# Performance work log

Measured on AMD Instinct MI355X. Metric: run time of the kernel, lower is better.

Reference implementation:

```python
import jax, jax.numpy as jnp
import numpy as np

NUM_HEADS = 32
NUM_KV_HEADS = 8
HEAD_DIM = 128
WINDOW = 512
NUM_META = 4


def _swa_sink_mask(S):
    # allowed = causal & (within sliding window OR sink/meta token)
    i = jnp.arange(S)[:, None]   # q_idx
    j = jnp.arange(S)[None, :]   # kv_idx
    return (i >= j) & (((i - j) <= WINDOW) | (j < NUM_META))


def setup_inputs() -> dict:
    key = jax.random.key(0)
    k1, k2, k3 = jax.random.split(key, 3)
    B, S = 1, 2048
    return {
        "query_states": jax.random.normal(k1, (B, S, NUM_HEADS * HEAD_DIM), dtype=jnp.float32),
        "key_states": jax.random.normal(k2, (B, S, NUM_KV_HEADS * HEAD_DIM), dtype=jnp.float32),
        "value_states": jax.random.normal(k3, (B, S, NUM_KV_HEADS * HEAD_DIM), dtype=jnp.float32),
    }


def reference(query_states, key_states, value_states):
    B, S, _ = query_states.shape
    n_rep = NUM_HEADS // NUM_KV_HEADS
    # [B, H, S, D]
    q = query_states.reshape(B, S, NUM_HEADS, HEAD_DIM).transpose(0, 2, 1, 3)
    k = key_states.reshape(B, S, NUM_KV_HEADS, HEAD_DIM).transpose(0, 2, 1, 3)
    v = value_states.reshape(B, S, NUM_KV_HEADS, HEAD_DIM).transpose(0, 2, 1, 3)
    # repeat_kv: interleaved repeat along head dim (GQA)
    k = jnp.repeat(k, n_rep, axis=1)
    v = jnp.repeat(v, n_rep, axis=1)

    scale = 1.0 / jnp.sqrt(jnp.float32(HEAD_DIM))  # flex_attention default scale
    scores = jnp.einsum("bhqd,bhkd->bhqk", q, k) * scale
    mask = _swa_sink_mask(S)  # [S, S], every row has q_idx==kv_idx allowed
    scores = jnp.where(mask[None, None], scores, -jnp.inf)
    attn = jax.nn.softmax(scores, axis=-1)
    out = jnp.einsum("bhqk,bhkd->bhqd", attn, v)
    return out.transpose(0, 2, 1, 3).reshape(B, S, NUM_HEADS * HEAD_DIM)
```

## Files before the change

### kernel.cpp

```cpp
#include <hip/hip_runtime.h>
#include <math.h>

typedef __attribute__((ext_vector_type(8))) short bf16x8;
typedef __attribute__((ext_vector_type(16))) float f32x16;

#define WIN 512
#define META 4
#define KSTR 136
#define VSTR 72
#define QSCALE (0.08838834764831845f * 1.4426950408889634f)
#define MFIX2 20.197730572445487f

union U8 { int4 i4; bf16x8 bf; };

static __device__ __forceinline__ unsigned bf16_rne(float x) {
  unsigned u = __float_as_uint(x);
  return (u + 0x7FFFu + ((u >> 16) & 1u)) >> 16;
}
static __device__ __forceinline__ unsigned pk2_rne(float a, float b) {
  return bf16_rne(a) | (bf16_rne(b) << 16);
}
static __device__ __forceinline__ unsigned pk2_tr(float a, float b) {
  return (__float_as_uint(a) >> 16) | (__float_as_uint(b) & 0xFFFF0000u);
}

__global__ __launch_bounds__(512, 2) void swa_fused(
    const float* __restrict__ Qg, const float* __restrict__ Kg,
    const float* __restrict__ Vg, float* __restrict__ Og)
{
  __shared__ __align__(16) unsigned short Ks[2][64 * KSTR];
  __shared__ __align__(16) unsigned short Vts[2][128 * VSTR];

  const int tid = threadIdx.x;
  const int lane = tid & 63, wid = tid >> 6;
  const int cl = lane & 31, hl = lane >> 5;
  const int bid = blockIdx.x;
  const int hk = bid & 7;
  const int bq = bid >> 3;
  const int q0 = bq << 6;
  const int h = hk * 4 + (wid & 3);
  const int qw0 = q0 + ((wid >> 2) << 5);

  const int ksh = tid >> 5;
  const int ksc = (tid & 31) * 4;
  const int dgv = tid & 31;
  const int kq = tid >> 5;
  const int vchunk = 2 * (kq >> 2) + (kq & 1);
  const int vhalf  = (kq >> 1) & 1;
  const int vxor   = (dgv >> 1) & 7;

  int4 qf[8];
  {
    const float* qrow = Qg + (size_t)(qw0 + cl) * 4096 + h * 128 + hl * 8;
    #pragma unroll
    for (int kc = 0; kc < 8; ++kc) {
      float4 x = *(const float4*)(qrow + kc * 16);
      float4 y = *(const float4*)(qrow + kc * 16 + 4);
      qf[kc] = make_int4(pk2_rne(x.x*QSCALE, x.y*QSCALE), pk2_rne(x.z*QSCALE, x.w*QSCALE),
                         pk2_rne(y.x*QSCALE, y.y*QSCALE), pk2_rne(y.z*QSCALE, y.w*QSCALE));
    }
  }

  f32x16 acc[4];
  #pragma unroll
  for (int nt = 0; nt < 4; ++nt)
    #pragma unroll
    for (int i = 0; i < 16; ++i) acc[nt][i] = 0.f;
  float lpA = 0.f, lpB = 0.f;

  const int jstart = (q0 > WIN) ? ((q0 - WIN) & ~63) : 0;
  const int sink = (jstart > 0) ? 1 : 0;
  const int niter = ((q0 + 63 - jstart) >> 6) + 1 + sink;

  float4 kreg[4], vreg[4];
  {
    const int jt0 = sink ? 0 : jstart;
    const float* kb = Kg + (size_t)jt0 * 1024 + hk * 128 + ksc;
    #pragma unroll
    for (int it = 0; it < 4; ++it)
      kreg[it] = *(const float4*)(kb + (size_t)(it * 16 + ksh) * 1024);
    const float* vb = Vg + (size_t)jt0 * 1024 + hk * 128 + dgv * 4;
    #pragma unroll
    for (int i = 0; i < 4; ++i)
      vreg[i] = *(const float4*)(vb + (size_t)(4 * kq + i) * 1024);
  }

  for (int t = 0; t < niter; ++t) {
    const bool isSink = (sink != 0) && (t == 0);
    const int jt = isSink ? 0 : jstart + ((t - sink) << 6);
    const bool needMask = (jt + 63 > qw0) || (qw0 + 31 - jt > WIN);
    const int cb = t & 1;
    unsigned short* Kb = Ks[cb];
    unsigned short* Vb = Vts[cb];

    #pragma unroll
    for (int it = 0; it < 4; ++it) {
      float4 v = kreg[it];
      *(uint2*)(Kb + (it * 16 + ksh) * KSTR + ksc) =
          make_uint2(pk2_tr(v.x, v.y), pk2_tr(v.z, v.w));
    }
    #pragma unroll
    for (int e = 0; e < 4; ++e) {
      const int d = dgv * 4 + e;
      const float* f0 = (const float*)&vreg[0];
      const float* f1 = (const float*)&vreg[1];
      const float* f2 = (const float*)&vreg[2];
      const float* f3 = (const float*)&vreg[3];
      *(uint2*)(Vb + d * VSTR + ((vchunk ^ vxor) << 3) + (vhalf << 2)) =
          make_uint2(pk2_tr(f0[e], f1[e]), pk2_tr(f2[e], f3[e]));
    }
    __syncthreads();

    if (t + 1 < niter) {
      const int jn = jstart + ((t + 1 - sink) << 6);
      const float* kb = Kg + (size_t)jn * 1024 + hk * 128 + ksc;
      #pragma unroll
      for (int it = 0; it < 4; ++it)
        kreg[it] = *(const float4*)(kb + (size_t)(it * 16 + ksh) * 1024);
      const float* vb = Vg + (size_t)jn * 1024 + hk * 128 + dgv * 4;
      #pragma unroll
      for (int i = 0; i < 4; ++i)
        vreg[i] = *(const float4*)(vb + (size_t)(4 * kq + i) * 1024);
    }

    f32x16 s0v, s1v;
    #pragma unroll
    for (int i = 0; i < 16; ++i) { s0v[i] = 0.f; s1v[i] = 0.f; }
    __builtin_amdgcn_s_setprio(1);
    if (isSink) {
      #pragma unroll
      for (int kc = 0; kc < 8; ++kc) {
        U8 b; b.i4 = qf[kc];
        U8 a0; a0.i4 = *(const int4*)(Kb + cl * KSTR + kc * 16 + hl * 8);
        s0v = __builtin_amdgcn_mfma_f32_32x32x16_bf16(a0.bf, b.bf, s0v, 0, 0, 0);
      }
    } else {
      #pragma unroll
      for (int kc = 0; kc < 8; ++kc) {
        U8 b; b.i4 = qf[kc];
        U8 a0; a0.i4 = *(const int4*)(Kb + cl * KSTR + kc * 16 + hl * 8);
        s0v = __builtin_amdgcn_mfma_f32_32x32x16_bf16(a0.bf, b.bf, s0v, 0, 0, 0);
        U8 a1; a1.i4 = *(const int4*)(Kb + (32 + cl) * KSTR + kc * 16 + hl * 8);
        s1v = __builtin_amdgcn_mfma_f32_32x32x16_bf16(a1.bf, b.bf, s1v, 0, 0, 0);
      }
    }
    __builtin_amdgcn_s_setprio(0);

    unsigned pu0[16], pu1[16];
    const int q = qw0 + cl;
    #pragma unroll
    for (int ri = 0; ri < 16; ++ri) {
      const int koff = (ri & 3) + 8 * (ri >> 2) + 4 * hl;
      bool ok0 = true, ok1 = true;
      if (needMask) {
        const int k0v = jt + koff, k1v = jt + 32 + koff;
        ok0 = (q >= k0v) && (((q - k0v) <= WIN) || (k0v < META));
        ok1 = (q >= k1v) && (((q - k1v) <= WIN) || (k1v < META));
      }
      unsigned u0 = ok0 ? (__float_as_uint(__builtin_amdgcn_exp2f(s0v[ri] - MFIX2)) & 0xFFFF0000u) : 0u;
      pu0[ri] = u0;
      lpA += __uint_as_float(u0);
      if (!isSink) {
        unsigned u1 = ok1 ? (__float_as_uint(__builtin_amdgcn_exp2f(s1v[ri] - MFIX2)) & 0xFFFF0000u) : 0u;
        pu1[ri] = u1;
        lpB += __uint_as_float(u1);
      }
    }

    #define MKA(P, o) make_int4((P[(o)] >> 16) | P[(o)+1], (P[(o)+2] >> 16) | P[(o)+3], \
                                (P[(o)+4] >> 16) | P[(o)+5], (P[(o)+6] >> 16) | P[(o)+7])
    const int kcmax = isSink ? 1 : 4;
    __builtin_amdgcn_s_setprio(1);
    for (int kc = 0; kc < kcmax; ++kc) {
      U8 a;
      a.i4 = (kc == 0) ? MKA(pu0, 0) : (kc == 1) ? MKA(pu0, 8)
           : (kc == 2) ? MKA(pu1, 0) : MKA(pu1, 8);
      #pragma unroll
      for (int nt = 0; nt < 4; ++nt) {
        const int dim = nt * 32 + cl;
        U8 b; b.i4 = *(const int4*)(Vb + dim * VSTR + (((2 * kc + hl) ^ ((dim >> 3) & 7)) << 3));
        acc[nt] = __builtin_amdgcn_mfma_f32_32x32x16_bf16(a.bf, b.bf, acc[nt], 0, 0, 0);
      }
    }
    __builtin_amdgcn_s_setprio(0);
    #undef MKA
  }

  const float lp = lpA + lpB;
  const float ltot = lp + __shfl_xor(lp, 32);
  const float inv = __fdividef(1.0f, ltot);
  #pragma unroll
  for (int ri = 0; ri < 16; ++ri) {
    const int rl = (ri & 3) + 8 * (ri >> 2) + 4 * hl;
    const float invq = __shfl(inv, rl, 64);
    #pragma unroll
    for (int nt = 0; nt < 4; ++nt) {
      Og[(size_t)(qw0 + rl) * 4096 + h * 128 + nt * 32 + cl] = acc[nt][ri] * invq;
    }
  }
}

extern "C" void kernel_launch(void* const* d_in, const int* in_sizes, int n_in,
                              void* d_out, int out_size, void* d_ws, size_t ws_size,
                              hipStream_t stream) {
  const float* Q = (const float*)d_in[0];
  const float* K = (const float*)d_in[1];
  const float* V = (const float*)d_in[2];
  float* O = (float*)d_out;
  hipLaunchKernelGGL(swa_fused, dim3(256), dim3(512), 0, stream, Q, K, V, O);
}
```

Measured before the change: 122.2 us.

## Defer second half of PV MFMAs into next iteration to overlap softmax

The P·V product for the second 32-key half of each tile is moved to the start of the following iteration. It reads the previous V buffer from the double-buffered LDS, and a tail block after the loop handles the last tile. The goal is to overlap these matrix-core ops with the next tile's LDS staging and exp work, hiding latency between the QK, softmax and PV phases. P packing also switches from shift-or to a single byte-permute instruction. In exchange, the pu1 registers must stay live across iterations, which raises register pressure.

```diff
diff --git a/kernel.cpp b/kernel.cpp
--- a/kernel.cpp
+++ b/kernel.cpp
@@ -85,6 +85,16 @@
       vreg[i] = *(const float4*)(vb + (size_t)(4 * kq + i) * 1024);
   }
 
+  #define MKA(P, o) make_int4( \
+      (int)__builtin_amdgcn_perm(P[(o)+1], P[(o)+0], 0x07060302u), \
+      (int)__builtin_amdgcn_perm(P[(o)+3], P[(o)+2], 0x07060302u), \
+      (int)__builtin_amdgcn_perm(P[(o)+5], P[(o)+4], 0x07060302u), \
+      (int)__builtin_amdgcn_perm(P[(o)+7], P[(o)+6], 0x07060302u))
+
+  unsigned pu1[16];
+  #pragma unroll
+  for (int i = 0; i < 16; ++i) pu1[i] = 0u;
+
   for (int t = 0; t < niter; ++t) {
     const bool isSink = (sink != 0) && (t == 0);
     const int jt = isSink ? 0 : jstart + ((t - sink) << 6);
@@ -92,6 +102,22 @@
     const int cb = t & 1;
     unsigned short* Kb = Ks[cb];
     unsigned short* Vb = Vts[cb];
+
+    if (t > sink) {
+      const unsigned short* Vp = Vts[cb ^ 1];
+      __builtin_amdgcn_s_setprio(1);
+      #pragma unroll
+      for (int kc = 2; kc < 4; ++kc) {
+        U8 a; a.i4 = (kc == 2) ? MKA(pu1, 0) : MKA(pu1, 8);
+        #pragma unroll
+        for (int nt = 0; nt < 4; ++nt) {
+          const int dim = nt * 32 + cl;
+          U8 b; b.i4 = *(const int4*)(Vp + dim * VSTR + (((2 * kc + hl) ^ ((dim >> 3) & 7)) << 3));
+          acc[nt] = __builtin_amdgcn_mfma_f32_32x32x16_bf16(a.bf, b.bf, acc[nt], 0, 0, 0);
+        }
+      }
+      __builtin_amdgcn_s_setprio(0);
+    }
 
     #pragma unroll
     for (int it = 0; it < 4; ++it) {
@@ -146,7 +172,7 @@
     }
     __builtin_amdgcn_s_setprio(0);
 
-    unsigned pu0[16], pu1[16];
+    unsigned pu0[16];
     const int q = qw0 + cl;
     #pragma unroll
     for (int ri = 0; ri < 16; ++ri) {
@@ -167,14 +193,11 @@
       }
     }
 
-    #define MKA(P, o) make_int4((P[(o)] >> 16) | P[(o)+1], (P[(o)+2] >> 16) | P[(o)+3], \
-                                (P[(o)+4] >> 16) | P[(o)+5], (P[(o)+6] >> 16) | P[(o)+7])
-    const int kcmax = isSink ? 1 : 4;
+    const int kcmax = isSink ? 1 : 2;
     __builtin_amdgcn_s_setprio(1);
     for (int kc = 0; kc < kcmax; ++kc) {
       U8 a;
-      a.i4 = (kc == 0) ? MKA(pu0, 0) : (kc == 1) ? MKA(pu0, 8)
-           : (kc == 2) ? MKA(pu1, 0) : MKA(pu1, 8);
+      a.i4 = (kc == 0) ? MKA(pu0, 0) : MKA(pu0, 8);
       #pragma unroll
       for (int nt = 0; nt < 4; ++nt) {
         const int dim = nt * 32 + cl;
@@ -183,8 +206,22 @@
       }
     }
     __builtin_amdgcn_s_setprio(0);
-    #undef MKA
-  }
+  }
+
+  {
+    const unsigned short* Vp = Vts[(niter - 1) & 1];
+    #pragma unroll
+    for (int kc = 2; kc < 4; ++kc) {
+      U8 a; a.i4 = (kc == 2) ? MKA(pu1, 0) : MKA(pu1, 8);
+      #pragma unroll
+      for (int nt = 0; nt < 4; ++nt) {
+        const int dim = nt * 32 + cl;
+        U8 b; b.i4 = *(const int4*)(Vp + dim * VSTR + (((2 * kc + hl) ^ ((dim >> 3) & 7)) << 3));
+        acc[nt] = __builtin_amdgcn_mfma_f32_32x32x16_bf16(a.bf, b.bf, acc[nt], 0, 0, 0);
+      }
+    }
+  }
+  #undef MKA
 
   const float lp = lpA + lpB;
   const float ltot = lp + __shfl_xor(lp, 32);
```

New measurement: 122.4 us. About the same (+0.1%).

## Use 128-key tiles with two substeps and defer last PV MFMAs across barrier

Applied to the files above, without the earlier changes.

Doubles the KV tile to 128 keys per shared-memory stage, cutting the number of barriers and global-load rounds in half. Each stage is processed as two 64-key substeps, and substeps that fall entirely outside the causal or sliding-window band are skipped. The last two P·V MFMA groups of each tile are deferred into the next iteration so they overlap the next tile's shared-memory stores. P packing switches to perm instructions. The cost is double the LDS footprint and more registers for the larger K/V prefetch buffers, which could limit occupancy.

```diff
diff --git a/kernel.cpp b/kernel.cpp
--- a/kernel.cpp
+++ b/kernel.cpp
@@ -7,7 +7,7 @@
 #define WIN 512
 #define META 4
 #define KSTR 136
-#define VSTR 72
+#define VSTR 136
 #define QSCALE (0.08838834764831845f * 1.4426950408889634f)
 #define MFIX2 20.197730572445487f
 
@@ -24,11 +24,12 @@
   return (__float_as_uint(a) >> 16) | (__float_as_uint(b) & 0xFFFF0000u);
 }
 
-__global__ __launch_bounds__(512, 2) void swa_fused(
-    const float* __restrict__ Qg, const float* __restrict__ Kg,
-    const float* __restrict__ Vg, float* __restrict__ Og)
+__global__ __attribute__((amdgpu_flat_work_group_size(512, 512)))
+__attribute__((amdgpu_waves_per_eu(2, 2)))
+void swa_fused(const float* __restrict__ Qg, const float* __restrict__ Kg,
+               const float* __restrict__ Vg, float* __restrict__ Og)
 {
-  __shared__ __align__(16) unsigned short Ks[2][64 * KSTR];
+  __shared__ __align__(16) unsigned short Ks[2][128 * KSTR];
   __shared__ __align__(16) unsigned short Vts[2][128 * VSTR];
 
   const int tid = threadIdx.x;
@@ -68,122 +69,167 @@
     for (int i = 0; i < 16; ++i) acc[nt][i] = 0.f;
   float lpA = 0.f, lpB = 0.f;
 
-  const int jstart = (q0 > WIN) ? ((q0 - WIN) & ~63) : 0;
+  const int jstart = (q0 > WIN) ? ((q0 - WIN) & ~127) : 0;
   const int sink = (jstart > 0) ? 1 : 0;
-  const int niter = ((q0 + 63 - jstart) >> 6) + 1 + sink;
-
-  float4 kreg[4], vreg[4];
+  const int ntile = (q0 + 64 - jstart + 127) >> 7;
+  const int niter = ntile + sink;
+
+  auto pv4 = [&](const unsigned short* Vh, const int hb, const int kc,
+                 unsigned w0, unsigned w1, unsigned w2, unsigned w3) {
+    U8 a; a.i4 = make_int4((int)w0, (int)w1, (int)w2, (int)w3);
+    #pragma unroll
+    for (int nt = 0; nt < 4; ++nt) {
+      const int dim = nt * 32 + cl;
+      U8 b; b.i4 = *(const int4*)(Vh + dim * VSTR +
+                    ((8 * hb + ((2 * kc + hl) ^ ((dim >> 3) & 7))) << 3));
+      acc[nt] = __builtin_amdgcn_mfma_f32_32x32x16_bf16(a.bf, b.bf, acc[nt], 0, 0, 0);
+    }
+  };
+
+  unsigned pkD[8];
+  #pragma unroll
+  for (int i = 0; i < 8; ++i) pkD[i] = 0u;
+
+  auto substep = [&](const int cb, const int jts, const int hb,
+                     const bool isS, const bool defer) -> bool {
+    if (jts > qw0 + 31) return false;
+    if ((jts + 63 < qw0 - WIN) && (jts >= META)) return false;
+    const bool needMask = (jts + 63 > qw0) || (qw0 + 31 - jts > WIN);
+    const unsigned short* Kh = &Ks[cb][hb * 64 * KSTR];
+    const unsigned short* Vh = &Vts[cb][0];
+
+    f32x16 s0v, s1v;
+    #pragma unroll
+    for (int i = 0; i < 16; ++i) { s0v[i] = 0.f; s1v[i] = 0.f; }
+    __builtin_amdgcn_s_setprio(1);
+    #pragma unroll
+    for (int kc = 0; kc < 8; ++kc) {
+      U8 b; b.i4 = qf[kc];
+      U8 a0; a0.i4 = *(const int4*)(Kh + cl * KSTR + kc * 16 + hl * 8);
+      s0v = __builtin_amdgcn_mfma_f32_32x32x16_bf16(a0.bf, b.bf, s0v, 0, 0, 0);
+      if (!isS) {
+        U8 a1; a1.i4 = *(const int4*)(Kh + (32 + cl) * KSTR + kc * 16 + hl * 8);
+        s1v = __builtin_amdgcn_mfma_f32_32x32x16_bf16(a1.bf, b.bf, s1v, 0, 0, 0);
+      }
+    }
+    __builtin_amdgcn_s_setprio(0);
+
+    unsigned pk0[8], pk1[8];
+    const int q = qw0 + cl;
+    #pragma unroll
+    for (int ri = 0; ri < 16; ri += 2) {
+      const int koff = (ri & 3) + 8 * (ri >> 2) + 4 * hl;
+      bool okE = true, okO = true, okE1 = true, okO1 = true;
+      if (needMask) {
+        const int kE = jts + koff;
+        okE  = (q >= kE)     && (((q - kE)     <= WIN) || (kE     < META));
+        okO  = (q >= kE + 1) && (((q - kE - 1) <= WIN) || (kE + 1 < META));
+        const int kF = kE + 32;
+        okE1 = (q >= kF)     && (((q - kF)     <= WIN) || (kF     < META));
+        okO1 = (q >= kF + 1) && (((q - kF - 1) <= WIN) || (kF + 1 < META));
+      }
+      unsigned uE = okE ? (__float_as_uint(__builtin_amdgcn_exp2f(s0v[ri]   - MFIX2)) & 0xFFFF0000u) : 0u;
+      unsigned uO = okO ? (__float_as_uint(__builtin_amdgcn_exp2f(s0v[ri+1] - MFIX2)) & 0xFFFF0000u) : 0u;
+      lpA += __uint_as_float(uE) + __uint_as_float(uO);
+      pk0[ri >> 1] = __builtin_amdgcn_perm(uO, uE, 0x07060302u);
+      if (!isS) {
+        unsigned vE = okE1 ? (__float_as_uint(__builtin_amdgcn_exp2f(s1v[ri]   - MFIX2)) & 0xFFFF0000u) : 0u;
+        unsigned vO = okO1 ? (__float_as_uint(__builtin_amdgcn_exp2f(s1v[ri+1] - MFIX2)) & 0xFFFF0000u) : 0u;
+        lpB += __uint_as_float(vE) + __uint_as_float(vO);
+        pk1[ri >> 1] = __builtin_amdgcn_perm(vO, vE, 0x07060302u);
+      }
+    }
+
+    __builtin_amdgcn_s_setprio(1);
+    pv4(Vh, hb, 0, pk0[0], pk0[1], pk0[2], pk0[3]);
+    if (!isS) {
+      pv4(Vh, hb, 1, pk0[4], pk0[5], pk0[6], pk0[7]);
+      if (!defer) {
+        pv4(Vh, hb, 2, pk1[0], pk1[1], pk1[2], pk1[3]);
+        pv4(Vh, hb, 3, pk1[4], pk1[5], pk1[6], pk1[7]);
+      } else {
+        #pragma unroll
+        for (int j = 0; j < 8; ++j) pkD[j] = pk1[j];
+      }
+    }
+    __builtin_amdgcn_s_setprio(0);
+    return true;
+  };
+
+  float4 kreg[8], vreg[8];
   {
     const int jt0 = sink ? 0 : jstart;
     const float* kb = Kg + (size_t)jt0 * 1024 + hk * 128 + ksc;
     #pragma unroll
-    for (int it = 0; it < 4; ++it)
+    for (int it = 0; it < 8; ++it)
       kreg[it] = *(const float4*)(kb + (size_t)(it * 16 + ksh) * 1024);
     const float* vb = Vg + (size_t)jt0 * 1024 + hk * 128 + dgv * 4;
     #pragma unroll
-    for (int i = 0; i < 4; ++i)
-      vreg[i] = *(const float4*)(vb + (size_t)(4 * kq + i) * 1024);
+    for (int i = 0; i < 8; ++i)
+      vreg[i] = *(const float4*)(vb + (size_t)((i >> 2) * 64 + 4 * kq + (i & 3)) * 1024);
   }
 
   for (int t = 0; t < niter; ++t) {
-    const bool isSink = (sink != 0) && (t == 0);
-    const int jt = isSink ? 0 : jstart + ((t - sink) << 6);
-    const bool needMask = (jt + 63 > qw0) || (qw0 + 31 - jt > WIN);
+    const bool isSinkT = (sink != 0) && (t == 0);
+    const int jt = isSinkT ? 0 : jstart + ((t - sink) << 7);
     const int cb = t & 1;
-    unsigned short* Kb = Ks[cb];
-    unsigned short* Vb = Vts[cb];
-
-    #pragma unroll
-    for (int it = 0; it < 4; ++it) {
+
+    if (t > sink) {
+      const unsigned short* Vp = &Vts[cb ^ 1][0];
+      __builtin_amdgcn_s_setprio(1);
+      pv4(Vp, 1, 2, pkD[0], pkD[1], pkD[2], pkD[3]);
+      pv4(Vp, 1, 3, pkD[4], pkD[5], pkD[6], pkD[7]);
+      __builtin_amdgcn_s_setprio(0);
+    }
+
+    #pragma unroll
+    for (int it = 0; it < 8; ++it) {
       float4 v = kreg[it];
-      *(uint2*)(Kb + (it * 16 + ksh) * KSTR + ksc) =
+      *(uint2*)(&Ks[cb][(it * 16 + ksh) * KSTR + ksc]) =
           make_uint2(pk2_tr(v.x, v.y), pk2_tr(v.z, v.w));
     }
     #pragma unroll
-    for (int e = 0; e < 4; ++e) {
-      const int d = dgv * 4 + e;
-      const float* f0 = (const float*)&vreg[0];
-      const float* f1 = (const float*)&vreg[1];
-      const float* f2 = (const float*)&vreg[2];
-      const float* f3 = (const float*)&vreg[3];
-      *(uint2*)(Vb + d * VSTR + ((vchunk ^ vxor) << 3) + (vhalf << 2)) =
-          make_uint2(pk2_tr(f0[e], f1[e]), pk2_tr(f2[e], f3[e]));
+    for (int hf = 0; hf < 2; ++hf) {
+      const float* f0 = (const float*)&vreg[hf * 4 + 0];
+      const float* f1 = (const float*)&vreg[hf * 4 + 1];
+      const float* f2 = (const float*)&vreg[hf * 4 + 2];
+      const float* f3 = (const float*)&vreg[hf * 4 + 3];
+      #pragma unroll
+      for (int e = 0; e < 4; ++e) {
+        const int d = dgv * 4 + e;
+        *(uint2*)(&Vts[cb][d * VSTR + ((8 * hf + (vchunk ^ vxor)) << 3) + (vhalf << 2)]) =
+            make_uint2(pk2_tr(f0[e], f1[e]), pk2_tr(f2[e], f3[e]));
+      }
     }
     __syncthreads();
 
     if (t + 1 < niter) {
-      const int jn = jstart + ((t + 1 - sink) << 6);
+      const int jn = jstart + ((t + 1 - sink) << 7);
       const float* kb = Kg + (size_t)jn * 1024 + hk * 128 + ksc;
       #pragma unroll
-      for (int it = 0; it < 4; ++it)
+      for (int it = 0; it < 8; ++it)
         kreg[it] = *(const float4*)(kb + (size_t)(it * 16 + ksh) * 1024);
       const float* vb = Vg + (size_t)jn * 1024 + hk * 128 + dgv * 4;
       #pragma unroll
-      for (int i = 0; i < 4; ++i)
-        vreg[i] = *(const float4*)(vb + (size_t)(4 * kq + i) * 1024);
-    }
-
-    f32x16 s0v, s1v;
-    #pragma unroll
-    for (int i = 0; i < 16; ++i) { s0v[i] = 0.f; s1v[i] = 0.f; }
-    __builtin_amdgcn_s_setprio(1);
-    if (isSink) {
-      #pragma unroll
-      for (int kc = 0; kc < 8; ++kc) {
-        U8 b; b.i4 = qf[kc];
-        U8 a0; a0.i4 = *(const int4*)(Kb + cl * KSTR + kc * 16 + hl * 8);
-        s0v = __builtin_amdgcn_mfma_f32_32x32x16_bf16(a0.bf, b.bf, s0v, 0, 0, 0);
-      }
+      for (int i = 0; i < 8; ++i)
+        vreg[i] = *(const float4*)(vb + (size_t)((i >> 2) * 64 + 4 * kq + (i & 3)) * 1024);
+    }
+
+    if (isSinkT) {
+      substep(cb, 0, 0, true, false);
     } else {
-      #pragma unroll
-      for (int kc = 0; kc < 8; ++kc) {
-        U8 b; b.i4 = qf[kc];
-        U8 a0; a0.i4 = *(const int4*)(Kb + cl * KSTR + kc * 16 + hl * 8);
-        s0v = __builtin_amdgcn_mfma_f32_32x32x16_bf16(a0.bf, b.bf, s0v, 0, 0, 0);
-        U8 a1; a1.i4 = *(const int4*)(Kb + (32 + cl) * KSTR + kc * 16 + hl * 8);
-        s1v = __builtin_amdgcn_mfma_f32_32x32x16_bf16(a1.bf, b.bf, s1v, 0, 0, 0);
-      }
-    }
-    __builtin_amdgcn_s_setprio(0);
-
-    unsigned pu0[16], pu1[16];
-    const int q = qw0 + cl;
-    #pragma unroll
-    for (int ri = 0; ri < 16; ++ri) {
-      const int koff = (ri & 3) + 8 * (ri >> 2) + 4 * hl;
-      bool ok0 = true, ok1 = true;
-      if (needMask) {
-        const int k0v = jt + koff, k1v = jt + 32 + koff;
-        ok0 = (q >= k0v) && (((q - k0v) <= WIN) || (k0v < META));
-        ok1 = (q >= k1v) && (((q - k1v) <= WIN) || (k1v < META));
-      }
-      unsigned u0 = ok0 ? (__float_as_uint(__builtin_amdgcn_exp2f(s0v[ri] - MFIX2)) & 0xFFFF0000u) : 0u;
-      pu0[ri] = u0;
-      lpA += __uint_as_float(u0);
-      if (!isSink) {
-        unsigned u1 = ok1 ? (__float_as_uint(__builtin_amdgcn_exp2f(s1v[ri] - MFIX2)) & 0xFFFF0000u) : 0u;
-        pu1[ri] = u1;
-        lpB += __uint_as_float(u1);
-      }
-    }
-
-    #define MKA(P, o) make_int4((P[(o)] >> 16) | P[(o)+1], (P[(o)+2] >> 16) | P[(o)+3], \
-                                (P[(o)+4] >> 16) | P[(o)+5], (P[(o)+6] >> 16) | P[(o)+7])
-    const int kcmax = isSink ? 1 : 4;
-    __builtin_amdgcn_s_setprio(1);
-    for (int kc = 0; kc < kcmax; ++kc) {
-      U8 a;
-      a.i4 = (kc == 0) ? MKA(pu0, 0) : (kc == 1) ? MKA(pu0, 8)
-           : (kc == 2) ? MKA(pu1, 0) : MKA(pu1, 8);
-      #pragma unroll
-      for (int nt = 0; nt < 4; ++nt) {
-        const int dim = nt * 32 + cl;
-        U8 b; b.i4 = *(const int4*)(Vb + dim * VSTR + (((2 * kc + hl) ^ ((dim >> 3) & 7)) << 3));
-        acc[nt] = __builtin_amdgcn_mfma_f32_32x32x16_bf16(a.bf, b.bf, acc[nt], 0, 0, 0);
-      }
-    }
-    __builtin_amdgcn_s_setprio(0);
-    #undef MKA
+      substep(cb, jt, 0, false, false);
+      if (!substep(cb, jt + 64, 1, false, true)) {
+        #pragma unroll
+        for (int j = 0; j < 8; ++j) pkD[j] = 0u;
+      }
+    }
+  }
+
+  {
+    const unsigned short* Vp = &Vts[(niter - 1) & 1][0];
+    pv4(Vp, 1, 2, pkD[0], pkD[1], pkD[2], pkD[3]);
+    pv4(Vp, 1, 3, pkD[4], pkD[5], pkD[6], pkD[7]);
   }
 
   const float lp = lpA + lpB;
```

After: 192.1 us. +57.2%, slower.

## Pre-convert K/V to bf16 tiles and stream them with async global-to-LDS loads

Applied to the files above, without the earlier changes.

A new prep kernel converts K and V from fp32 to bf16 once, writing them in MFMA-ready tiled layouts in workspace. The attention kernel then copies these tiles straight into LDS with global_load_lds, so it no longer does register round-trips or per-block conversion. It also adds a third V buffer so the second half of each P·V product is deferred to the next iteration, overlapping it with the next loads. The cost is an extra kernel launch plus a workspace write and read of the converted K/V.

```diff
diff --git a/kernel.cpp b/kernel.cpp
--- a/kernel.cpp
+++ b/kernel.cpp
@@ -6,8 +6,6 @@
 
 #define WIN 512
 #define META 4
-#define KSTR 136
-#define VSTR 72
 #define QSCALE (0.08838834764831845f * 1.4426950408889634f)
 #define MFIX2 20.197730572445487f
 
@@ -23,13 +21,62 @@
 static __device__ __forceinline__ unsigned pk2_tr(float a, float b) {
   return (__float_as_uint(a) >> 16) | (__float_as_uint(b) & 0xFFFF0000u);
 }
+static __device__ __forceinline__ void gload16(const void* g, void* l) {
+  __builtin_amdgcn_global_load_lds(
+      (const __attribute__((address_space(1))) unsigned int*)g,
+      (__attribute__((address_space(3))) unsigned int*)l, 16, 0, 0);
+}
+
+__global__ __launch_bounds__(256) void swa_prep(
+    const float* __restrict__ Kg, const float* __restrict__ Vg,
+    unsigned short* __restrict__ Kw, unsigned short* __restrict__ Vw)
+{
+  __shared__ float Kf[64][132];
+  __shared__ float Vf[64][132];
+  const int tid = threadIdx.x;
+  const int hk = blockIdx.x & 7, tj = blockIdx.x >> 3;
+  const int j0 = tj * 64;
+  const int krow = tid >> 5;
+  const int f4c = tid & 31;
+  #pragma unroll
+  for (int r = 0; r < 8; ++r) {
+    const int key = r * 8 + krow;
+    *(float4*)&Kf[key][f4c * 4] =
+        *(const float4*)(Kg + (size_t)(j0 + key) * 1024 + hk * 128 + f4c * 4);
+    *(float4*)&Vf[key][f4c * 4] =
+        *(const float4*)(Vg + (size_t)(j0 + key) * 1024 + hk * 128 + f4c * 4);
+  }
+  __syncthreads();
+  unsigned short* kout = Kw + ((size_t)(hk * 32 + tj)) * 8192;
+  #pragma unroll
+  for (int p = 0; p < 4; ++p) {
+    const int gid = p * 256 + tid;
+    const int s = gid >> 6, key = gid & 63;
+    const float* src = &Kf[key][s * 8];
+    *(int4*)(kout + gid * 8) = make_int4(
+        (int)pk2_tr(src[0], src[1]), (int)pk2_tr(src[2], src[3]),
+        (int)pk2_tr(src[4], src[5]), (int)pk2_tr(src[6], src[7]));
+  }
+  unsigned short* vout = Vw + ((size_t)(hk * 32 + tj)) * 8192;
+  #pragma unroll
+  for (int p = 0; p < 4; ++p) {
+    const int fid = p * 256 + tid;
+    const int c = fid >> 7, dim = fid & 127;
+    const int kb = 16 * (c >> 1) + 4 * (c & 1);
+    *(int4*)(vout + fid * 8) = make_int4(
+        (int)pk2_tr(Vf[kb + 0][dim], Vf[kb + 1][dim]),
+        (int)pk2_tr(Vf[kb + 2][dim], Vf[kb + 3][dim]),
+        (int)pk2_tr(Vf[kb + 8][dim], Vf[kb + 9][dim]),
+        (int)pk2_tr(Vf[kb + 10][dim], Vf[kb + 11][dim]));
+  }
+}
 
 __global__ __launch_bounds__(512, 2) void swa_fused(
-    const float* __restrict__ Qg, const float* __restrict__ Kg,
-    const float* __restrict__ Vg, float* __restrict__ Og)
+    const float* __restrict__ Qg, const unsigned short* __restrict__ Kw,
+    const unsigned short* __restrict__ Vw, float* __restrict__ Og)
 {
-  __shared__ __align__(16) unsigned short Ks[2][64 * KSTR];
-  __shared__ __align__(16) unsigned short Vts[2][128 * VSTR];
+  __shared__ __align__(16) unsigned short KsB[2][8192];
+  __shared__ __align__(16) unsigned short VtB[3][8192];
 
   const int tid = threadIdx.x;
   const int lane = tid & 63, wid = tid >> 6;
@@ -41,14 +88,6 @@
   const int h = hk * 4 + (wid & 3);
   const int qw0 = q0 + ((wid >> 2) << 5);
 
-  const int ksh = tid >> 5;
-  const int ksc = (tid & 31) * 4;
-  const int dgv = tid & 31;
-  const int kq = tid >> 5;
-  const int vchunk = 2 * (kq >> 2) + (kq & 1);
-  const int vhalf  = (kq >> 1) & 1;
-  const int vxor   = (dgv >> 1) & 7;
-
   int4 qf[8];
   {
     const float* qrow = Qg + (size_t)(qw0 + cl) * 4096 + h * 128 + hl * 8;
@@ -71,56 +110,56 @@
   const int jstart = (q0 > WIN) ? ((q0 - WIN) & ~63) : 0;
   const int sink = (jstart > 0) ? 1 : 0;
   const int niter = ((q0 + 63 - jstart) >> 6) + 1 + sink;
-
-  float4 kreg[4], vreg[4];
-  {
-    const int jt0 = sink ? 0 : jstart;
-    const float* kb = Kg + (size_t)jt0 * 1024 + hk * 128 + ksc;
-    #pragma unroll
-    for (int it = 0; it < 4; ++it)
-      kreg[it] = *(const float4*)(kb + (size_t)(it * 16 + ksh) * 1024);
-    const float* vb = Vg + (size_t)jt0 * 1024 + hk * 128 + dgv * 4;
-    #pragma unroll
-    for (int i = 0; i < 4; ++i)
-      vreg[i] = *(const float4*)(vb + (size_t)(4 * kq + i) * 1024);
-  }
+  const int tj0 = jstart >> 6;
+
+  auto stage = [&](const int tj, unsigned short* kd, unsigned short* vd) {
+    const size_t base = ((size_t)(hk * 32 + tj)) << 14;
+    const char* ks = (const char*)Kw + base + tid * 16;
+    gload16(ks, (char*)kd + tid * 16);
+    gload16(ks + 8192, (char*)kd + tid * 16 + 8192);
+    const char* vs = (const char*)Vw + base + tid * 16;
+    gload16(vs, (char*)vd + tid * 16);
+    gload16(vs + 8192, (char*)vd + tid * 16 + 8192);
+  };
+
+  #define MKA(P, o) make_int4( \
+      (int)__builtin_amdgcn_perm(P[(o)+1], P[(o)+0], 0x07060302u), \
+      (int)__builtin_amdgcn_perm(P[(o)+3], P[(o)+2], 0x07060302u), \
+      (int)__builtin_amdgcn_perm(P[(o)+5], P[(o)+4], 0x07060302u), \
+      (int)__builtin_amdgcn_perm(P[(o)+7], P[(o)+6], 0x07060302u))
+
+  auto pv4 = [&](const unsigned short* Vb, const int kc, const int4 aw) {
+    U8 a; a.i4 = aw;
+    #pragma unroll
+    for (int nt = 0; nt < 4; ++nt) {
+      U8 b; b.i4 = *(const int4*)(Vb + kc * 2048 + hl * 1024 + nt * 256 + cl * 8);
+      acc[nt] = __builtin_amdgcn_mfma_f32_32x32x16_bf16(a.bf, b.bf, acc[nt], 0, 0, 0);
+    }
+  };
+
+  unsigned pu1[16];
+  #pragma unroll
+  for (int i = 0; i < 16; ++i) pu1[i] = 0u;
+
+  stage(sink ? 0 : tj0, KsB[0], VtB[0]);
+  __syncthreads();
+
+  const unsigned short *kCur = KsB[0], *kNxt = KsB[1];
+  const unsigned short *vPrv = VtB[2], *vCur = VtB[0], *vNxt = VtB[1];
 
   for (int t = 0; t < niter; ++t) {
     const bool isSink = (sink != 0) && (t == 0);
     const int jt = isSink ? 0 : jstart + ((t - sink) << 6);
     const bool needMask = (jt + 63 > qw0) || (qw0 + 31 - jt > WIN);
-    const int cb = t & 1;
-    unsigned short* Kb = Ks[cb];
-    unsigned short* Vb = Vts[cb];
-
-    #pragma unroll
-    for (int it = 0; it < 4; ++it) {
-      float4 v = kreg[it];
-      *(uint2*)(Kb + (it * 16 + ksh) * KSTR + ksc) =
-          make_uint2(pk2_tr(v.x, v.y), pk2_tr(v.z, v.w));
-    }
-    #pragma unroll
-    for (int e = 0; e < 4; ++e) {
-      const int d = dgv * 4 + e;
-      const float* f0 = (const float*)&vreg[0];
-      const float* f1 = (const float*)&vreg[1];
-      const float* f2 = (const float*)&vreg[2];
-      const float* f3 = (const float*)&vreg[3];
-      *(uint2*)(Vb + d * VSTR + ((vchunk ^ vxor) << 3) + (vhalf << 2)) =
-          make_uint2(pk2_tr(f0[e], f1[e]), pk2_tr(f2[e], f3[e]));
-    }
-    __syncthreads();
-
-    if (t + 1 < niter) {
-      const int jn = jstart + ((t + 1 - sink) << 6);
-      const float* kb = Kg + (size_t)jn * 1024 + hk * 128 + ksc;
-      #pragma unroll
-      for (int it = 0; it < 4; ++it)
-        kreg[it] = *(const float4*)(kb + (size_t)(it * 16 + ksh) * 1024);
-      const float* vb = Vg + (size_t)jn * 1024 + hk * 128 + dgv * 4;
-      #pragma unroll
-      for (int i = 0; i < 4; ++i)
-        vreg[i] = *(const float4*)(vb + (size_t)(4 * kq + i) * 1024);
+
+    if (t + 1 < niter)
+      stage(tj0 + (t + 1 - sink), (unsigned short*)kNxt, (unsigned short*)vNxt);
+
+    if (t > sink) {
+      __builtin_amdgcn_s_setprio(1);
+      pv4(vPrv, 2, MKA(pu1, 0));
+      pv4(vPrv, 3, MKA(pu1, 8));
+      __builtin_amdgcn_s_setprio(0);
     }
 
     f32x16 s0v, s1v;
@@ -131,22 +170,22 @@
       #pragma unroll
       for (int kc = 0; kc < 8; ++kc) {
         U8 b; b.i4 = qf[kc];
-        U8 a0; a0.i4 = *(const int4*)(Kb + cl * KSTR + kc * 16 + hl * 8);
+        U8 a0; a0.i4 = *(const int4*)(kCur + kc * 1024 + hl * 512 + cl * 8);
         s0v = __builtin_amdgcn_mfma_f32_32x32x16_bf16(a0.bf, b.bf, s0v, 0, 0, 0);
       }
     } else {
       #pragma unroll
       for (int kc = 0; kc < 8; ++kc) {
         U8 b; b.i4 = qf[kc];
-        U8 a0; a0.i4 = *(const int4*)(Kb + cl * KSTR + kc * 16 + hl * 8);
+        U8 a0; a0.i4 = *(const int4*)(kCur + kc * 1024 + hl * 512 + cl * 8);
         s0v = __builtin_amdgcn_mfma_f32_32x32x16_bf16(a0.bf, b.bf, s0v, 0, 0, 0);
-        U8 a1; a1.i4 = *(const int4*)(Kb + (32 + cl) * KSTR + kc * 16 + hl * 8);
+        U8 a1; a1.i4 = *(const int4*)(kCur + kc * 1024 + hl * 512 + 256 + cl * 8);
         s1v = __builtin_amdgcn_mfma_f32_32x32x16_bf16(a1.bf, b.bf, s1v, 0, 0, 0);
       }
     }
     __builtin_amdgcn_s_setprio(0);
 
-    unsigned pu0[16], pu1[16];
+    unsigned pu0[16];
     const int q = qw0 + cl;
     #pragma unroll
     for (int ri = 0; ri < 16; ++ri) {
@@ -167,24 +206,20 @@
       }
     }
 
-    #define MKA(P, o) make_int4((P[(o)] >> 16) | P[(o)+1], (P[(o)+2] >> 16) | P[(o)+3], \
-                                (P[(o)+4] >> 16) | P[(o)+5], (P[(o)+6] >> 16) | P[(o)+7])
-    const int kcmax = isSink ? 1 : 4;
     __builtin_amdgcn_s_setprio(1);
-    for (int kc = 0; kc < kcmax; ++kc) {
-      U8 a;
-      a.i4 = (kc == 0) ? MKA(pu0, 0) : (kc == 1) ? MKA(pu0, 8)
-           : (kc == 2) ? MKA(pu1, 0) : MKA(pu1, 8);
-      #pragma unroll
-      for (int nt = 0; nt < 4; ++nt) {
-        const int dim = nt * 32 + cl;
-        U8 b; b.i4 = *(const int4*)(Vb + dim * VSTR + (((2 * kc + hl) ^ ((dim >> 3) & 7)) << 3));
-        acc[nt] = __builtin_amdgcn_mfma_f32_32x32x16_bf16(a.bf, b.bf, acc[nt], 0, 0, 0);
-      }
-    }
+    pv4(vCur, 0, MKA(pu0, 0));
+    if (!isSink) pv4(vCur, 1, MKA(pu0, 8));
     __builtin_amdgcn_s_setprio(0);
-    #undef MKA
-  }
+
+    __syncthreads();
+
+    { const unsigned short* tk = kCur; kCur = kNxt; kNxt = tk; }
+    { const unsigned short* tv = vPrv; vPrv = vCur; vCur = vNxt; vNxt = tv; }
+  }
+
+  pv4(vPrv, 2, MKA(pu1, 0));
+  pv4(vPrv, 3, MKA(pu1, 8));
+  #undef MKA
 
   const float lp = lpA + lpB;
   const float ltot = lp + __shfl_xor(lp, 32);
@@ -207,5 +242,8 @@
   const float* K = (const float*)d_in[1];
   const float* V = (const float*)d_in[2];
   float* O = (float*)d_out;
-  hipLaunchKernelGGL(swa_fused, dim3(256), dim3(512), 0, stream, Q, K, V, O);
-}
+  unsigned short* Kw = (unsigned short*)d_ws;
+  unsigned short* Vw = Kw + (size_t)8 * 32 * 8192;
+  hipLaunchKernelGGL(swa_prep, dim3(256), dim3(256), 0, stream, K, V, Kw, Vw);
+  hipLaunchKernelGGL(swa_fused, dim3(256), dim3(512), 0, stream, Q, Kw, Vw, O);
+}
```

After: 123.4 us. Within noise of the previous version (+1.0%).
